# Kernel tuning notes

Hardware: AMD Instinct MI355X
Metric: run time of the kernel (lower is better)

Reference implementation:

```python
import jax, jax.numpy as jnp
import numpy as np

# Cubic B-spline blending matrix (rows give cumulative weights w0,w1,w2)
_B_SPLINE = np.array([[5., 3., -3., 1.],
                      [1., 3., 3., -2.],
                      [0., 0., 0., 1.]], dtype=np.float32) / 6.0


def _hat(w):
    # w: [..., 3] -> skew-symmetric [..., 3, 3]
    x, y, z = w[..., 0], w[..., 1], w[..., 2]
    o = jnp.zeros_like(x)
    return jnp.stack([jnp.stack([o, -z, y], -1),
                      jnp.stack([z, o, -x], -1),
                      jnp.stack([-y, x, o], -1)], -2)


def _se3_exp(xi):
    # xi: [..., 6] = [nu (trans), omega (rot)] -> homogeneous [..., 4, 4]
    nu, om = xi[..., :3], xi[..., 3:]
    th2 = jnp.sum(om * om, axis=-1)
    small = th2 < 1e-8
    th = jnp.sqrt(jnp.where(small, 1.0, th2))  # grad-safe sqrt
    A = jnp.where(small, 1.0 - th2 / 6.0, jnp.sin(th) / th)
    Bc = jnp.where(small, 0.5 - th2 / 24.0, (1.0 - jnp.cos(th)) / th2)
    C = jnp.where(small, 1.0 / 6.0 - th2 / 120.0, (th - jnp.sin(th)) / (th2 * th))
    H = _hat(om)
    H2 = H @ H
    I = jnp.eye(3, dtype=xi.dtype)
    R = I + A[..., None, None] * H + Bc[..., None, None] * H2
    V = I + Bc[..., None, None] * H + C[..., None, None] * H2
    t = jnp.einsum('...ij,...j->...i', V, nu)
    top = jnp.concatenate([R, t[..., None]], axis=-1)          # [..., 3, 4]
    bot = jnp.zeros_like(top[..., :1, :]).at[..., 0, 3].set(1.0)  # [..., 1, 4]
    return jnp.concatenate([top, bot], axis=-2)


def _se3_log_Rt(R, t):
    # (R,t) -> se3 twist [..., 6] = [V^{-1} t, omega]
    tr = R[..., 0, 0] + R[..., 1, 1] + R[..., 2, 2]
    cos_th = jnp.clip(0.5 * (tr - 1.0), -1.0 + 1e-6, 1.0 - 1e-6)
    th = jnp.arccos(cos_th)
    vee = 0.5 * jnp.stack([R[..., 2, 1] - R[..., 1, 2],
                           R[..., 0, 2] - R[..., 2, 0],
                           R[..., 1, 0] - R[..., 0, 1]], axis=-1)
    omega = (th / jnp.sin(th))[..., None] * vee
    th2 = th * th
    small = th < 5e-2
    th_s = jnp.where(small, 1.0, th)
    D = jnp.where(small,
                  1.0 / 12.0 + th2 / 720.0,
                  1.0 / (th_s * th_s) - (1.0 + cos_th) / (2.0 * th_s * jnp.sin(th_s)))
    H = _hat(omega)
    Vinv = jnp.eye(3, dtype=R.dtype) - 0.5 * H + D[..., None, None] * (H @ H)
    nu = jnp.einsum('...ij,...j->...i', Vinv, t)
    return jnp.concatenate([nu, omega], axis=-1)


def _rel_log(Ta, Tb):
    # log( inv(Ta) @ Tb ) without materializing the inverse
    Ra, pa = Ta[..., :3, :3], Ta[..., :3, 3]
    Rb, pb = Tb[..., :3, :3], Tb[..., :3, 3]
    R = jnp.einsum('...ji,...jk->...ik', Ra, Rb)
    t = jnp.einsum('...ji,...j->...i', Ra, pb - pa)
    return _se3_log_Rt(R, t)


def setup_inputs() -> dict:
    key = jax.random.key(0)
    k1, k2, k3 = jax.random.split(key, 3)
    Bsz, n, K = 32, 512, 64
    trans = jax.random.normal(k1, (Bsz, n, 3), dtype=jnp.float32) * 2.0
    rot = jax.random.normal(k2, (Bsz, n, 3), dtype=jnp.float32) * 0.3
    input_poses = _se3_exp(jnp.concatenate([trans, rot], axis=-1))  # valid SE3
    time = jax.random.uniform(k3, (1, 1, K), dtype=jnp.float32)
    return {"input_poses": input_poses, "time": time}


def reference(input_poses, time):
    dtype = input_poses.dtype
    # duplicate begin & end control poses (inter_begin_and_end=True)
    poses = jnp.concatenate([input_poses[:, :1], input_poses, input_poses[:, -1:]], axis=1)
    Bsz = poses.shape[0]
    P = poses.shape[1] - 3  # number of spline segments
    tvec = time.reshape(-1)  # [k]
    K = tvec.shape[0]
    powers = jnp.stack([jnp.ones_like(tvec), tvec, tvec * tvec, tvec ** 3], axis=0)  # [4,k]
    w = jnp.asarray(_B_SPLINE, dtype) @ powers  # [3, k]

    T0 = poses[:, :-3]   # [B, P, 4, 4]
    T1 = poses[:, 1:-2]
    T2 = poses[:, 2:-1]
    T3 = poses[:, 3:]

    xi01 = _rel_log(T0, T1)  # [B, P, 6]
    xi12 = _rel_log(T1, T2)
    xi23 = _rel_log(T2, T3)

    # weight each twist per time sample, then exp-map: [B, P, k, 4, 4]
    A0 = _se3_exp(w[0][None, None, :, None] * xi01[:, :, None, :])
    A1 = _se3_exp(w[1][None, None, :, None] * xi12[:, :, None, :])
    A2 = _se3_exp(w[2][None, None, :, None] * xi23[:, :, None, :])

    waypoints = T0[:, :, None] @ A0 @ A1 @ A2  # [B, P, k, 4, 4]
    return waypoints.reshape(Bsz, P * K, 4, 4)
```

## Files before the change

kernel.cpp:

```cpp
#include <hip/hip_runtime.h>
#include <hip/hip_bf16.h>


__device__ __forceinline__ float frcp(float x) { return __builtin_amdgcn_rcpf(x); }

using f32x4 = __attribute__((ext_vector_type(4))) float;

struct Quat { float w, x, y, z; };

__device__ __forceinline__ void rel_log(const float* __restrict__ Ta,
                                        const float* __restrict__ Tb,
                                        float xi[6]) {
    float R[9];
#pragma unroll
    for (int i = 0; i < 3; ++i)
#pragma unroll
        for (int j = 0; j < 3; ++j)
            R[i * 3 + j] = Ta[0 * 4 + i] * Tb[0 * 4 + j] +
                           Ta[1 * 4 + i] * Tb[1 * 4 + j] +
                           Ta[2 * 4 + i] * Tb[2 * 4 + j];
    float dx = Tb[3] - Ta[3], dy = Tb[7] - Ta[7], dz = Tb[11] - Ta[11];
    float t0 = Ta[0] * dx + Ta[4] * dy + Ta[8] * dz;
    float t1 = Ta[1] * dx + Ta[5] * dy + Ta[9] * dz;
    float t2 = Ta[2] * dx + Ta[6] * dy + Ta[10] * dz;

    float tr = R[0] + R[4] + R[8];
    float cos_th = 0.5f * (tr - 1.0f);
    cos_th = fminf(fmaxf(cos_th, -1.0f + 1e-6f), 1.0f - 1e-6f);
    float th = acosf(cos_th);
    float s = sinf(th);
    float vx = 0.5f * (R[7] - R[5]);
    float vy = 0.5f * (R[2] - R[6]);
    float vz = 0.5f * (R[3] - R[1]);
    float f = th / s;
    float ox = f * vx, oy = f * vy, oz = f * vz;
    float th2 = th * th;
    float D;
    if (th < 0.05f)
        D = 1.0f / 12.0f + th2 / 720.0f;
    else
        D = 1.0f / th2 - (1.0f + cos_th) / (2.0f * th * s);

    float oo = ox * ox + oy * oy + oz * oz;
    float V00 = 1.0f + D * (ox * ox - oo);
    float V01 = 0.5f * oz + D * (ox * oy);
    float V02 = -0.5f * oy + D * (ox * oz);
    float V10 = -0.5f * oz + D * (ox * oy);
    float V11 = 1.0f + D * (oy * oy - oo);
    float V12 = 0.5f * ox + D * (oy * oz);
    float V20 = 0.5f * oy + D * (ox * oz);
    float V21 = -0.5f * ox + D * (oy * oz);
    float V22 = 1.0f + D * (oz * oz - oo);

    xi[0] = V00 * t0 + V01 * t1 + V02 * t2;
    xi[1] = V10 * t0 + V11 * t1 + V12 * t2;
    xi[2] = V20 * t0 + V21 * t1 + V22 * t2;
    xi[3] = ox; xi[4] = oy; xi[5] = oz;
}

__global__ void __launch_bounds__(256)
rel_log_kernel(const float* __restrict__ poses, float* __restrict__ rel,
               int n, int total) {
    int idx = blockIdx.x * blockDim.x + threadIdx.x;
    if (idx >= total) return;
    int m = n + 1;
    int j = idx % m;
    int b = idx / m;
    int ia = max(j - 1, 0);
    int ib = min(j, n - 1);
    const float* base = poses + (size_t)b * n * 16;
    float xi[6];
    rel_log(base + ia * 16, base + ib * 16, xi);
    float4* o4 = (float4*)(rel + (size_t)idx * 8);
    o4[0] = make_float4(xi[0], xi[1], xi[2], xi[3]);
    o4[1] = make_float4(xi[4], xi[5], 0.0f, 0.0f);
}

__device__ __forceinline__ void exp_qt(float wgt, const float* __restrict__ xi,
                                       Quat& q, float t[3]) {
    float nx = wgt * xi[0], ny = wgt * xi[1], nz = wgt * xi[2];
    float ox = wgt * xi[3], oy = wgt * xi[4], oz = wgt * xi[5];
    float th2 = ox * ox + oy * oy + oz * oz;
    bool small = th2 < 1e-8f;
    float th = sqrtf(th2);
    float rth = frcp(th);
    float sh, ch;
    __sincosf(0.5f * th, &sh, &ch);
    float rth2 = rth * rth;
    float sh2 = sh * sh;
    float sinth = 2.0f * sh * ch;
    float sfac = small ? 0.5f - th2 * (1.0f / 48.0f) : sh * rth;
    float B = small ? 0.5f - th2 * (1.0f / 24.0f) : (sh2 + sh2) * rth2;
    float C = small ? (1.0f / 6.0f) - th2 * (1.0f / 120.0f)
                    : (th - sinth) * rth2 * rth;
    q.w = ch; q.x = sfac * ox; q.y = sfac * oy; q.z = sfac * oz;
    float c1x = oy * nz - oz * ny;
    float c1y = oz * nx - ox * nz;
    float c1z = ox * ny - oy * nx;
    float c2x = oy * c1z - oz * c1y;
    float c2y = oz * c1x - ox * c1z;
    float c2z = ox * c1y - oy * c1x;
    t[0] = nx + B * c1x + C * c2x;
    t[1] = ny + B * c1y + C * c2y;
    t[2] = nz + B * c1z + C * c2z;
}

__device__ __forceinline__ Quat qmul(const Quat& a, const Quat& b) {
    Quat r;
    r.w = a.w * b.w - a.x * b.x - a.y * b.y - a.z * b.z;
    r.x = a.w * b.x + a.x * b.w + a.y * b.z - a.z * b.y;
    r.y = a.w * b.y - a.x * b.z + a.y * b.w + a.z * b.x;
    r.z = a.w * b.z + a.x * b.y - a.y * b.x + a.z * b.w;
    return r;
}

__device__ __forceinline__ void qrot(const Quat& q, const float v[3], float o[3]) {
    float ux = q.y * v[2] - q.z * v[1];
    float uy = q.z * v[0] - q.x * v[2];
    float uz = q.x * v[1] - q.y * v[0];
    float sx = q.w * ux + (q.y * uz - q.z * uy);
    float sy = q.w * uy + (q.z * ux - q.x * uz);
    float sz = q.w * uz + (q.x * uy - q.y * ux);
    o[0] = v[0] + 2.0f * sx;
    o[1] = v[1] + 2.0f * sy;
    o[2] = v[2] + 2.0f * sz;
}

__device__ __forceinline__ void q2m(const Quat& q, float M[9]) {
    float x2 = q.x + q.x, y2 = q.y + q.y, z2 = q.z + q.z;
    float xx = q.x * x2, yy = q.y * y2, zz = q.z * z2;
    float xy = q.x * y2, xz = q.x * z2, yz = q.y * z2;
    float wx = q.w * x2, wy = q.w * y2, wz = q.w * z2;
    M[0] = 1.0f - (yy + zz); M[1] = xy - wz;          M[2] = xz + wy;
    M[3] = xy + wz;          M[4] = 1.0f - (xx + zz); M[5] = yz - wx;
    M[6] = xz - wy;          M[7] = yz + wx;          M[8] = 1.0f - (xx + yy);
}

__global__ void __launch_bounds__(256)
spline_eval_k64(const float* __restrict__ poses,
                const float* __restrict__ rel,
                const float* __restrict__ timev,
                float* __restrict__ out,
                int n, int total) {
    __shared__ f32x4 lds4[768];

    int tid = threadIdx.x;
    int g = blockIdx.x * 256 + tid;
    bool fullBlock = (blockIdx.x + 1) * 256 <= total;
    bool active = g < total;

    f32x4 r0, r1, r2;
    if (active) {
        int k = g & 63;
        int bp = __builtin_amdgcn_readfirstlane(g >> 6);
        int P = n - 1;
        int p = bp % P;
        int b = bp / P;
        int m = n + 1;

        const float* xs = rel + (size_t)(b * m + p) * 8;
        const float* T0 = poses + ((size_t)b * n + max(p - 1, 0)) * 16;

        float tt = timev[k];
        float t2 = tt * tt, t3 = t2 * tt;
        float w0 = (5.0f + 3.0f * tt - 3.0f * t2 + t3) * (1.0f / 6.0f);
        float w1 = (1.0f + 3.0f * tt + 3.0f * t2 - 2.0f * t3) * (1.0f / 6.0f);
        float w2 = t3 * (1.0f / 6.0f);

        Quat qa, qb, qc;
        float ta[3], tb[3], tc[3];
        exp_qt(w0, xs + 0, qa, ta);
        exp_qt(w1, xs + 8, qb, tb);
        exp_qt(w2, xs + 16, qc, tc);

        Quat qabc = qmul(qmul(qa, qb), qc);

        float u[3], v[3];
        qrot(qb, tc, u);
        u[0] += tb[0]; u[1] += tb[1]; u[2] += tb[2];
        qrot(qa, u, v);
        v[0] += ta[0]; v[1] += ta[1]; v[2] += ta[2];

        float M[9];
        q2m(qabc, M);

        float o[12];
#pragma unroll
        for (int i = 0; i < 3; ++i) {
            float a0 = T0[4 * i + 0], a1 = T0[4 * i + 1], a2 = T0[4 * i + 2];
            o[4 * i + 0] = a0 * M[0] + a1 * M[3] + a2 * M[6];
            o[4 * i + 1] = a0 * M[1] + a1 * M[4] + a2 * M[7];
            o[4 * i + 2] = a0 * M[2] + a1 * M[5] + a2 * M[8];
            o[4 * i + 3] = T0[4 * i + 3] + a0 * v[0] + a1 * v[1] + a2 * v[2];
        }
        r0 = (f32x4){o[0], o[1], o[2], o[3]};
        r1 = (f32x4){o[4], o[5], o[6], o[7]};
        r2 = (f32x4){o[8], o[9], o[10], o[11]};
    }

    if (fullBlock) {
        lds4[0 * 256 + tid] = r0;
        lds4[1 * 256 + tid] = r1;
        lds4[2 * 256 + tid] = r2;
        __syncthreads();
        f32x4* outb = (f32x4*)out + (size_t)blockIdx.x * 1024;
        int r = tid & 3;
        int a = tid >> 2;
        const f32x4 last = (f32x4){0.0f, 0.0f, 0.0f, 1.0f};
#pragma unroll
        for (int i = 0; i < 4; ++i) {
            f32x4 val = (r == 3) ? last : lds4[r * 256 + 64 * i + a];
            __builtin_nontemporal_store(val, &outb[i * 256 + tid]);
        }
    } else if (active) {
        f32x4* o4 = (f32x4*)(out + (size_t)g * 16);
        o4[0] = r0;
        o4[1] = r1;
        o4[2] = r2;
        o4[3] = (f32x4){0.0f, 0.0f, 0.0f, 1.0f};
    }
}

__device__ __forceinline__ void se3_exp_scaled(float sc, const float xi[6],
                                               float R[9], float t[3]) {
    float nx = sc * xi[0], ny = sc * xi[1], nz = sc * xi[2];
    float ox = sc * xi[3], oy = sc * xi[4], oz = sc * xi[5];
    float th2 = ox * ox + oy * oy + oz * oz;
    float A, B, C;
    if (th2 < 1e-8f) {
        A = 1.0f - th2 * (1.0f / 6.0f);
        B = 0.5f - th2 * (1.0f / 24.0f);
        C = 1.0f / 6.0f - th2 * (1.0f / 120.0f);
    } else {
        float th = sqrtf(th2);
        float sn, cs;
        __sincosf(th, &sn, &cs);
        float r = frcp(th);
        float r2 = r * r;
        A = sn * r;
        B = (1.0f - cs) * r2;
        C = (th - sn) * r2 * r;
    }
    float xx = ox * ox, yy = oy * oy, zz = oz * oz;
    float xy = ox * oy, xz = ox * oz, yz = oy * oz;
    R[0] = 1.0f + B * (xx - th2);
    R[1] = B * xy - A * oz;
    R[2] = B * xz + A * oy;
    R[3] = B * xy + A * oz;
    R[4] = 1.0f + B * (yy - th2);
    R[5] = B * yz - A * ox;
    R[6] = B * xz - A * oy;
    R[7] = B * yz + A * ox;
    R[8] = 1.0f + B * (zz - th2);
    float V00 = 1.0f + C * (xx - th2);
    float V01 = C * xy - B * oz;
    float V02 = C * xz + B * oy;
    float V10 = C * xy + B * oz;
    float V11 = 1.0f + C * (yy - th2);
    float V12 = C * yz - B * ox;
    float V20 = C * xz - B * oy;
    float V21 = C * yz + B * ox;
    float V22 = 1.0f + C * (zz - th2);
    t[0] = V00 * nx + V01 * ny + V02 * nz;
    t[1] = V10 * nx + V11 * ny + V12 * nz;
    t[2] = V20 * nx + V21 * ny + V22 * nz;
}

__device__ __forceinline__ void compose(const float R1[9], const float t1[3],
                                        const float R2[9], const float t2[3],
                                        float Ro[9], float to[3]) {
#pragma unroll
    for (int i = 0; i < 3; ++i) {
#pragma unroll
        for (int j = 0; j < 3; ++j)
            Ro[i * 3 + j] = R1[i * 3 + 0] * R2[0 * 3 + j] +
                            R1[i * 3 + 1] * R2[1 * 3 + j] +
                            R1[i * 3 + 2] * R2[2 * 3 + j];
        to[i] = R1[i * 3 + 0] * t2[0] + R1[i * 3 + 1] * t2[1] +
                R1[i * 3 + 2] * t2[2] + t1[i];
    }
}

__global__ void __launch_bounds__(256)
lie_spline_mono(const float* __restrict__ poses,
                const float* __restrict__ timev,
                float* __restrict__ out,
                int n, int K, int total) {
    int g = blockIdx.x * blockDim.x + threadIdx.x;
    if (g >= total) return;
    int P = n - 1;
    int k = g % K;
    int bp = g / K;
    int p = bp % P;
    int b = bp / P;
    int i0 = max(p - 1, 0);
    int i1 = p;
    int i2 = min(p + 1, n - 1);
    int i3 = min(p + 2, n - 1);
    const float* base = poses + (size_t)b * n * 16;
    const float *T0 = base + i0 * 16, *T1 = base + i1 * 16;
    const float *T2 = base + i2 * 16, *T3 = base + i3 * 16;
    float xi01[6], xi12[6], xi23[6];
    rel_log(T0, T1, xi01);
    rel_log(T1, T2, xi12);
    rel_log(T2, T3, xi23);
    float t = timev[k];
    float t2 = t * t, t3 = t2 * t;
    float w0 = (5.0f + 3.0f * t - 3.0f * t2 + t3) * (1.0f / 6.0f);
    float w1 = (1.0f + 3.0f * t + 3.0f * t2 - 2.0f * t3) * (1.0f / 6.0f);
    float w2 = t3 * (1.0f / 6.0f);
    float Ra[9], ta[3], Rb[9], tb[3], Rc[9], tc[3];
    se3_exp_scaled(w0, xi01, Ra, ta);
    se3_exp_scaled(w1, xi12, Rb, tb);
    se3_exp_scaled(w2, xi23, Rc, tc);
    float R0[9] = {T0[0], T0[1], T0[2], T0[4], T0[5], T0[6], T0[8], T0[9], T0[10]};
    float p0[3] = {T0[3], T0[7], T0[11]};
    float Rx[9], tx[3], Ry[9], ty[3], Rz[9], tz[3];
    compose(R0, p0, Ra, ta, Rx, tx);
    compose(Rx, tx, Rb, tb, Ry, ty);
    compose(Ry, ty, Rc, tc, Rz, tz);
    float4* o4 = (float4*)(out + (size_t)g * 16);
    o4[0] = make_float4(Rz[0], Rz[1], Rz[2], tz[0]);
    o4[1] = make_float4(Rz[3], Rz[4], Rz[5], tz[1]);
    o4[2] = make_float4(Rz[6], Rz[7], Rz[8], tz[2]);
    o4[3] = make_float4(0.0f, 0.0f, 0.0f, 1.0f);
}

extern "C" void kernel_launch(void* const* d_in, const int* in_sizes, int n_in,
                              void* d_out, int out_size, void* d_ws, size_t ws_size,
                              hipStream_t stream) {
    const float* poses = (const float*)d_in[0];
    const float* timev = (const float*)d_in[1];
    float* out = (float*)d_out;

    int K = in_sizes[1];
    int S = in_sizes[0] / 16;
    int Q = out_size / (16 * K);
    int Bsz = S - Q;
    int n = S / Bsz;

    int P = n - 1;
    int total = Bsz * P * K;
    int block = 256;

    size_t rel_bytes = (size_t)Bsz * (n + 1) * 8 * sizeof(float);
    if (K == 64 && ws_size >= rel_bytes) {
        float* rel = (float*)d_ws;
        int total1 = Bsz * (n + 1);
        hipLaunchKernelGGL(rel_log_kernel, dim3((total1 + block - 1) / block),
                           dim3(block), 0, stream, poses, rel, n, total1);
        hipLaunchKernelGGL(spline_eval_k64, dim3((total + block - 1) / block),
                           dim3(block), 0, stream, poses, rel, timev, out,
                           n, total);
    } else {
        hipLaunchKernelGGL(lie_spline_mono, dim3((total + block - 1) / block),
                           dim3(block), 0, stream, poses, timev, out,
                           n, K, total);
    }
}
```

Before: 27.63 us.

## Fuse relative-log precompute into spline evaluation kernel, dropping workspace pass

After: 34.88 us. +26.2%, slower.

```diff
diff --git a/kernel.cpp b/kernel.cpp
--- a/kernel.cpp
+++ b/kernel.cpp
@@ -56,24 +56,6 @@
     xi[1] = V10 * t0 + V11 * t1 + V12 * t2;
     xi[2] = V20 * t0 + V21 * t1 + V22 * t2;
     xi[3] = ox; xi[4] = oy; xi[5] = oz;
-}
-
-__global__ void __launch_bounds__(256)
-rel_log_kernel(const float* __restrict__ poses, float* __restrict__ rel,
-               int n, int total) {
-    int idx = blockIdx.x * blockDim.x + threadIdx.x;
-    if (idx >= total) return;
-    int m = n + 1;
-    int j = idx % m;
-    int b = idx / m;
-    int ia = max(j - 1, 0);
-    int ib = min(j, n - 1);
-    const float* base = poses + (size_t)b * n * 16;
-    float xi[6];
-    rel_log(base + ia * 16, base + ib * 16, xi);
-    float4* o4 = (float4*)(rel + (size_t)idx * 8);
-    o4[0] = make_float4(xi[0], xi[1], xi[2], xi[3]);
-    o4[1] = make_float4(xi[4], xi[5], 0.0f, 0.0f);
 }
 
 __device__ __forceinline__ void exp_qt(float wgt, const float* __restrict__ xi,
@@ -137,11 +119,10 @@
 }
 
 __global__ void __launch_bounds__(256)
-spline_eval_k64(const float* __restrict__ poses,
-                const float* __restrict__ rel,
-                const float* __restrict__ timev,
-                float* __restrict__ out,
-                int n, int total) {
+spline_fused_k64(const float* __restrict__ poses,
+                 const float* __restrict__ timev,
+                 float* __restrict__ out,
+                 int n, int total) {
     __shared__ f32x4 lds4[768];
 
     int tid = threadIdx.x;
@@ -156,10 +137,20 @@
         int P = n - 1;
         int p = bp % P;
         int b = bp / P;
-        int m = n + 1;
-
-        const float* xs = rel + (size_t)(b * m + p) * 8;
-        const float* T0 = poses + ((size_t)b * n + max(p - 1, 0)) * 16;
+
+        int i0 = max(p - 1, 0);
+        int i2 = min(p + 1, n - 1);
+        int i3 = min(p + 2, n - 1);
+        const float* base = poses + (size_t)b * n * 16;
+        const float* T0 = base + i0 * 16;
+        const float* T1 = base + p * 16;
+        const float* T2 = base + i2 * 16;
+        const float* T3 = base + i3 * 16;
+
+        float xi01[6], xi12[6], xi23[6];
+        rel_log(T0, T1, xi01);
+        rel_log(T1, T2, xi12);
+        rel_log(T2, T3, xi23);
 
         float tt = timev[k];
         float t2 = tt * tt, t3 = t2 * tt;
@@ -169,9 +160,9 @@
 
         Quat qa, qb, qc;
         float ta[3], tb[3], tc[3];
-        exp_qt(w0, xs + 0, qa, ta);
-        exp_qt(w1, xs + 8, qb, tb);
-        exp_qt(w2, xs + 16, qc, tc);
+        exp_qt(w0, xi01, qa, ta);
+        exp_qt(w1, xi12, qb, tb);
+        exp_qt(w2, xi23, qc, tc);
 
         Quat qabc = qmul(qmul(qa, qb), qc);
 
@@ -343,14 +334,9 @@
     int total = Bsz * P * K;
     int block = 256;
 
-    size_t rel_bytes = (size_t)Bsz * (n + 1) * 8 * sizeof(float);
-    if (K == 64 && ws_size >= rel_bytes) {
-        float* rel = (float*)d_ws;
-        int total1 = Bsz * (n + 1);
-        hipLaunchKernelGGL(rel_log_kernel, dim3((total1 + block - 1) / block),
-                           dim3(block), 0, stream, poses, rel, n, total1);
-        hipLaunchKernelGGL(spline_eval_k64, dim3((total + block - 1) / block),
-                           dim3(block), 0, stream, poses, rel, timev, out,
+    if (K == 64) {
+        hipLaunchKernelGGL(spline_fused_k64, dim3((total + block - 1) / block),
+                           dim3(block), 0, stream, poses, timev, out,
                            n, total);
     } else {
         hipLaunchKernelGGL(lie_spline_mono, dim3((total + block - 1) / block),
```
